# Performance work log

Hardware: AMD Instinct MI355X
Metric: run time of the kernel (lower is better)

Reference implementation:

```python
import jax, jax.numpy as jnp
import numpy as np

B, L, DIM = 4, 2048, 512
H, D = 8, 64
SCALE = D ** -0.5
NEG = -10000.0


def setup_inputs() -> dict:
    key = jax.random.key(0)
    ks = jax.random.split(key, 5)
    std = 1.0 / np.sqrt(DIM)
    return {
        "x": jax.random.normal(ks[0], (B, L, DIM), dtype=jnp.float32),
        "wq": jax.random.normal(ks[1], (H * D, DIM), dtype=jnp.float32) * std,
        "wk": jax.random.normal(ks[2], (H * D, DIM), dtype=jnp.float32) * std,
        "wv": jax.random.normal(ks[3], (H * D, DIM), dtype=jnp.float32) * std,
        "wo": jax.random.normal(ks[4], (DIM, H * D), dtype=jnp.float32) * std,
    }


def reference(x, wq, wk, wv, wo):
    b, l, _ = x.shape
    # projections (torch Linear: y = x @ W.T), split heads -> [b,h,l,d]
    q = (x @ wq.T).reshape(b, l, H, D).transpose(0, 2, 1, 3)
    k = (x @ wk.T).reshape(b, l, H, D).transpose(0, 2, 1, 3)
    v = (x @ wv.T).reshape(b, l, H, D).transpose(0, 2, 1, 3)
    scores = jnp.einsum("bhld,bhsd->bhls", q, k) * SCALE
    scores = jnp.nan_to_num(scores, nan=0.0, posinf=10000.0, neginf=NEG)
    diag = jnp.eye(l, dtype=bool)[None, None]  # [1,1,l,l]
    scores = jnp.where(diag, NEG, scores)
    attn = jax.nn.softmax(scores, axis=-1)
    attn = jnp.where(diag, 0.0, attn)
    attn = jnp.nan_to_num(attn, nan=0.0, posinf=0.0, neginf=0.0)
    out = jnp.einsum("bhls,bhsd->bhld", attn, v)
    out = out.transpose(0, 2, 1, 3).reshape(b, l, H * D)
    return out @ wo.T
```

## Files before the change

### kernel.cpp

```cpp
#include <hip/hip_runtime.h>
#include <hip/hip_bf16.h>


#define Bsz 4
#define Lsz 2048
#define DIMsz 512
#define Hsz 8
#define Dsz 64

typedef _Float16 f16;
typedef __attribute__((ext_vector_type(8))) _Float16 f16x8;
typedef __attribute__((ext_vector_type(4))) _Float16 f16x4;
typedef __attribute__((ext_vector_type(2))) __fp16 fp16x2;
typedef __attribute__((ext_vector_type(4))) float f32x4;
typedef __attribute__((ext_vector_type(16))) float f32x16;
typedef unsigned int u32;
typedef __attribute__((ext_vector_type(2))) unsigned int u32x2;

#if __has_builtin(__builtin_amdgcn_exp2f)
#define EXP2(x) __builtin_amdgcn_exp2f(x)
#else
#define EXP2(x) __expf(0.6931471805599453f * (x))
#endif

__device__ __forceinline__ u32 pack2(float a, float b) {
#if __has_builtin(__builtin_amdgcn_cvt_pkrtz)
    fp16x2 h = __builtin_amdgcn_cvt_pkrtz(a, b);
    return __builtin_bit_cast(u32, h);
#else
    fp16x2 h; h.x = (__fp16)a; h.y = (__fp16)b;
    return __builtin_bit_cast(u32, h);
#endif
}

#if __has_builtin(__builtin_amdgcn_permlane32_swap)
__device__ __forceinline__ void plswap(u32& a, u32& b) {
    u32x2 r = __builtin_amdgcn_permlane32_swap(a, b, false, false);
    a = r.x; b = r.y;
}
#else
__device__ __forceinline__ void plswap(u32& a, u32& b) {
    u32 sa = (u32)__shfl_xor((int)a, 32);
    u32 sb = (u32)__shfl_xor((int)b, 32);
    bool hi = (threadIdx.x & 32) != 0;
    u32 na = hi ? sb : a;
    u32 nb = hi ? b : sa;
    a = na; b = nb;
}
#endif

__device__ __forceinline__ void gl2lds16(const void* g, void* l) {
    __builtin_amdgcn_global_load_lds(
        (const __attribute__((address_space(1))) u32*)g,
        (__attribute__((address_space(3))) u32*)l, 16, 0, 0);
}

__global__ __launch_bounds__(256) void pack_f16(
    const float* __restrict__ x, const float* __restrict__ wq,
    const float* __restrict__ wk, const float* __restrict__ wv,
    const float* __restrict__ wo,
    f16* __restrict__ xh, f16* __restrict__ w3h, f16* __restrict__ woh)
{
    int bx = blockIdx.x, seg, blk;
    if (bx < 4096) { seg = 0; blk = bx; }
    else { seg = 1 + ((bx - 4096) >> 8); blk = (bx - 4096) & 255; }
    const float* s; f16* d; float sc = 1.0f;
    switch (seg) {
        case 0: s = x;  d = xh;            break;
        case 1: s = wq; d = w3h;           sc = 0.18033688011112042f; break;
        case 2: s = wk; d = w3h + 262144;  break;
        case 3: s = wv; d = w3h + 524288;  break;
        default: s = wo; d = woh;          break;
    }
    int i = (blk * 256 + threadIdx.x) * 4;
    float4 v = *(const float4*)(s + i);
    f16x4 o;
    o.x = (f16)(v.x * sc); o.y = (f16)(v.y * sc);
    o.z = (f16)(v.z * sc); o.w = (f16)(v.w * sc);
    *(f16x4*)(d + i) = o;
}

__global__ __launch_bounds__(256) void gemm_qkv_f16(
    const f16* __restrict__ A, const f16* __restrict__ B,
    f16* __restrict__ qh, f16* __restrict__ kh, f16* __restrict__ vth)
{
    __shared__ __align__(16) char smem[32768];
    f16* Ash = (f16*)smem;
    f16* Bsh = (f16*)(smem + 16384);

    const int tid = threadIdx.x;
    const int w = tid >> 6, lane = tid & 63;
    const int quad = lane >> 4, low = lane & 15;
    const int wm = w >> 1, wn = w & 1;
    const int m0 = blockIdx.y * 128, n0 = blockIdx.x * 128;

    f32x4 acc[4][4];
    #pragma unroll
    for (int i = 0; i < 4; i++)
        #pragma unroll
        for (int j = 0; j < 4; j++) acc[i][j] = (f32x4){0.f, 0.f, 0.f, 0.f};

    #pragma unroll 1
    for (int k0 = 0; k0 < DIMsz; k0 += 64) {
        __syncthreads();
        #pragma unroll
        for (int j = 0; j < 4; j++) {
            int t = j * 256 + tid;
            int r = t >> 3, g = t & 7;
            int gc = (g ^ (r & 7)) * 8;
            char* lb = (char*)Ash + (j * 256 + w * 64) * 16;
            gl2lds16(A + (size_t)(m0 + r) * DIMsz + k0 + gc, lb);
            char* lb2 = (char*)Bsh + (j * 256 + w * 64) * 16;
            gl2lds16(B + (size_t)(n0 + r) * DIMsz + k0 + gc, lb2);
        }
        __syncthreads();

        #pragma unroll
        for (int ks2 = 0; ks2 < 2; ks2++) {
            f16x8 af[4], bf[4];
            #pragma unroll
            for (int mt = 0; mt < 4; mt++) {
                int ar = wm * 64 + mt * 16 + low;
                int c = ks2 * 4 + quad;
                af[mt] = *(const f16x8*)&Ash[ar * 64 + ((c ^ (ar & 7)) << 3)];
            }
            #pragma unroll
            for (int nt = 0; nt < 4; nt++) {
                int br = wn * 64 + nt * 16 + low;
                int c = ks2 * 4 + quad;
                bf[nt] = *(const f16x8*)&Bsh[br * 64 + ((c ^ (br & 7)) << 3)];
            }
            #pragma unroll
            for (int mt = 0; mt < 4; mt++)
                #pragma unroll
                for (int nt = 0; nt < 4; nt++)
                    acc[mt][nt] = __builtin_amdgcn_mfma_f32_16x16x32_f16(
                        af[mt], bf[nt], acc[mt][nt], 0, 0, 0);
        }
    }

    const int proj = n0 >> 9;
    const int b_ = m0 >> 11, l0 = m0 & (Lsz - 1);
    if (proj < 2) {
        f16* dst = (proj == 0) ? qh : kh;
        f16* Tq = (f16*)smem;
        const int hb = (n0 & 511) >> 6;
        #pragma unroll 1
        for (int hs = 0; hs < 2; hs++) {
            __syncthreads();
            if (wn == hs) {
                #pragma unroll
                for (int nt = 0; nt < 4; nt++) {
                    int cl = nt * 16 + low;
                    #pragma unroll
                    for (int mt = 0; mt < 4; mt++)
                        #pragma unroll
                        for (int r = 0; r < 4; r++) {
                            int l = wm * 64 + mt * 16 + quad * 4 + r;
                            Tq[l * 72 + cl] = (f16)acc[mt][nt][r];
                        }
                }
            }
            __syncthreads();
            int l = tid >> 1, d0 = (tid & 1) * 32;
            size_t bhh = (size_t)(b_ * Hsz + hb + hs);
            f16* dstp = dst + (bhh * Lsz + l0 + l) * Dsz + d0;
            const f16* srcp = Tq + l * 72 + d0;
            #pragma unroll
            for (int j = 0; j < 4; j++)
                *(f16x8*)(dstp + j * 8) = *(const f16x8*)(srcp + j * 8);
        }
    } else {
        const int hb = (n0 & 511) >> 6;
        f16* Tv = (f16*)smem;
        #pragma unroll 1
        for (int hs = 0; hs < 2; hs++) {
            __syncthreads();
            if (wn == hs) {
                #pragma unroll
                for (int nt = 0; nt < 4; nt++) {
                    int d = nt * 16 + low;
                    #pragma unroll
                    for (int mt = 0; mt < 4; mt++)
                        #pragma unroll
                        for (int r = 0; r < 4; r++) {
                            int l = wm * 64 + mt * 16 + quad * 4 + r;
                            Tv[d * 136 + l] = (f16)acc[mt][nt][r];
                        }
                }
            }
            __syncthreads();
            int d = tid >> 2, seg = tid & 3;
            size_t bh = (size_t)(b_ * Hsz + hb + hs);
            f16* dstp = vth + (bh * 64 + d) * (size_t)Lsz + l0 + seg * 32;
            const f16* srcp = Tv + d * 136 + seg * 32;
            #pragma unroll
            for (int j = 0; j < 4; j++)
                *(f16x8*)(dstp + j * 8) = *(const f16x8*)(srcp + j * 8);
        }
    }
}

__global__ __launch_bounds__(256, 4) void attn_mfma(
    const f16* __restrict__ q, const f16* __restrict__ k,
    const f16* __restrict__ vt, f16* __restrict__ ctx)
{
    __shared__ __align__(16) char smem[33792];

    const int tid = threadIdx.x;
    const int w = tid >> 6, lane = tid & 63;
    const int col = lane & 31;
    const int h = lane >> 5;
    const int kw = w & 1, qw = w >> 1;
    const int bh = blockIdx.x;
    const int qb = blockIdx.y;
    const int q0 = qb * 64;
    const size_t kvb = (size_t)bh * Lsz;

    f16* Ks = (f16*)smem;
    f16* Vs = (f16*)(smem + 16384);

    f16x8 qf[4];
    #pragma unroll
    for (int s = 0; s < 4; s++)
        qf[s] = *(const f16x8*)(q + (kvb + q0 + qw * 32 + col) * Dsz
                                  + s * 16 + h * 8);
    #pragma unroll
    for (int s = 0; s < 4; s++)
        asm volatile("" :: "v"(qf[s]));

    const f16* kp; const f16* vp;
    {
        int r8 = tid >> 3, g8 = tid & 7;
        int gc = (g8 ^ (r8 & 7) ^ ((r8 >> 3) & 3)) << 3;
        kp = k + (kvb + r8) * Dsz + gc;
        vp = vt + ((size_t)bh * Dsz + r8) * Lsz + gc;
    }
    char* kl = (char*)smem + w * 1024;
    char* vl = (char*)smem + 16384 + w * 1024;

    const int cswz = (col & 7) ^ ((col >> 3) & 3);
    const f16* kfp[4];
    #pragma unroll
    for (int s = 0; s < 4; s++)
        kfp[s] = Ks + (kw * 32 + col) * 64 + (((s * 2 + h) ^ cswz) << 3);
    const f16* vfp[2][2];
    #pragma unroll
    for (int dt = 0; dt < 2; dt++)
        #pragma unroll
        for (int ks = 0; ks < 2; ks++) {
            int cv = kw * 4 + ks * 2 + h;
            vfp[dt][ks] = Vs + (dt * 32 + col) * 64 + ((cv ^ cswz) << 3);
        }

    f32x16 acc[2];
    #pragma unroll
    for (int dt = 0; dt < 2; dt++)
        #pragma unroll
        for (int i = 0; i < 16; i++) acc[dt][i] = 0.f;
    float lsum = 0.f;

    gl2lds16(kp,            kl);
    gl2lds16(kp + 32 * Dsz, kl + 4096);
    gl2lds16(vp,            vl);
    gl2lds16(vp + 32 * Lsz, vl + 4096);
    kp += 64 * Dsz;
    vp += 64;

#define ATTN_ROUND(S0, P, PRE) do {                                           \
    const int ko_ = (P) * 8192;                                               \
    if (PRE) {                                                                \
        const int nx_ = ((P) ^ 1) * 8192;                                     \
        gl2lds16(kp,            kl + nx_);                                    \
        gl2lds16(kp + 32 * Dsz, kl + nx_ + 4096);                             \
        gl2lds16(vp,            vl + nx_);                                    \
        gl2lds16(vp + 32 * Lsz, vl + nx_ + 4096);                             \
        kp += 64 * Dsz;                                                       \
        vp += 64;                                                             \
        asm volatile("s_waitcnt vmcnt(4)" ::: "memory");                      \
    } else {                                                                  \
        asm volatile("s_waitcnt vmcnt(0)" ::: "memory");                      \
    }                                                                         \
    __builtin_amdgcn_s_barrier();                                             \
    __builtin_amdgcn_sched_barrier(0);                                        \
      \
    f32x16 st;                                                                \
    _Pragma("unroll")                                                         \
    for (int i = 0; i < 16; i++) st[i] = 0.f;                                 \
    __builtin_amdgcn_s_setprio(1);                                            \
    _Pragma("unroll")                                                         \
    for (int s = 0; s < 4; s++) {                                             \
        f16x8 kf = *(const f16x8*)((const char*)kfp[s] + ko_);                \
        st = __builtin_amdgcn_mfma_f32_32x32x16_f16(kf, qf[s], st, 0, 0, 0);  \
    }                                                                         \
    __builtin_amdgcn_s_setprio(0);                                            \
                \
    _Pragma("unroll")                                                         \
    for (int i = 0; i < 16; i++) st[i] = EXP2(st[i]);                         \
    if ((S0) == q0 && kw == qw) {                                             \
        _Pragma("unroll")                                                     \
        for (int i = 0; i < 16; i++) {                                        \
            int row = (i & 3) + 8 * (i >> 2) + 4 * h;                         \
            st[i] = (row == col) ? 0.f : st[i];                               \
        }                                                                     \
    }                                                                         \
    _Pragma("unroll")                                                         \
    for (int i = 0; i < 16; i++) lsum += st[i];                               \
                                                \
    u32 P2[8];                                                                \
    _Pragma("unroll")                                                         \
    for (int j = 0; j < 8; j++)                                               \
        P2[j] = pack2(st[2 * j], st[2 * j + 1]);                              \
    plswap(P2[0], P2[2]); plswap(P2[1], P2[3]);                               \
    plswap(P2[4], P2[6]); plswap(P2[5], P2[7]);                               \
    union { u32 u[4]; f16x8 v; } pfa, pfb;                                    \
    _Pragma("unroll")                                                         \
    for (int jj = 0; jj < 4; jj++) {                                          \
        pfa.u[jj] = P2[jj];                                                   \
        pfb.u[jj] = P2[4 + jj];                                               \
    }                                                                         \
                               \
    __builtin_amdgcn_s_setprio(1);                                            \
    _Pragma("unroll")                                                         \
    for (int dt = 0; dt < 2; dt++) {                                          \
        f16x8 vf0 = *(const f16x8*)((const char*)vfp[dt][0] + ko_);           \
        acc[dt] = __builtin_amdgcn_mfma_f32_32x32x16_f16(                     \
            vf0, pfa.v, acc[dt], 0, 0, 0);                                    \
        f16x8 vf1 = *(const f16x8*)((const char*)vfp[dt][1] + ko_);           \
        acc[dt] = __builtin_amdgcn_mfma_f32_32x32x16_f16(                     \
            vf1, pfb.v, acc[dt], 0, 0, 0);                                    \
    }                                                                         \
    __builtin_amdgcn_s_setprio(0);                                            \
    __builtin_amdgcn_sched_barrier(0);                                        \
    __builtin_amdgcn_s_barrier();                                             \
} while (0)

    #pragma unroll 1
    for (int s0 = 0; s0 < Lsz; s0 += 128) {
        ATTN_ROUND(s0, 0, true);
        ATTN_ROUND(s0 + 64, 1, (s0 + 128 < Lsz));
    }
#undef ATTN_ROUND

    __syncthreads();

    float* Lsp = (float*)(smem + 32768);
    lsum += __shfl_xor(lsum, 32);
    if (h == 0) Lsp[qw * 64 + kw * 32 + col] = lsum;

    float* Om = (float*)smem;
    if (kw == 1) {
        float* og = Om + qw * 2048;
        #pragma unroll
        for (int dt = 0; dt < 2; dt++)
            #pragma unroll
            for (int i = 0; i < 16; i++) {
                int row = (i & 3) + 8 * (i >> 2) + 4 * h;
                og[(dt * 32 + row) * 32 + col] = acc[dt][i];
            }
    }
    __syncthreads();
    if (kw == 0) {
        const float* og = Om + qw * 2048;
        #pragma unroll
        for (int dt = 0; dt < 2; dt++)
            #pragma unroll
            for (int i = 0; i < 16; i++) {
                int row = (i & 3) + 8 * (i >> 2) + 4 * h;
                acc[dt][i] += og[(dt * 32 + row) * 32 + col];
            }
        const int b = bh >> 3, hh = bh & 7;
        float ls = Lsp[qw * 64 + col] + Lsp[qw * 64 + 32 + col];
        const float inv = 1.0f / ls;
        f16* op = ctx + ((size_t)(b * Lsz + q0 + qw * 32 + col)) * DIMsz
                      + hh * 64;
        #pragma unroll
        for (int dt = 0; dt < 2; dt++)
            #pragma unroll
            for (int r4 = 0; r4 < 4; r4++) {
                f16x4 o;
                o.x = (f16)(acc[dt][4 * r4 + 0] * inv);
                o.y = (f16)(acc[dt][4 * r4 + 1] * inv);
                o.z = (f16)(acc[dt][4 * r4 + 2] * inv);
                o.w = (f16)(acc[dt][4 * r4 + 3] * inv);
                *(f16x4*)(op + dt * 32 + 8 * r4 + 4 * h) = o;
            }
    }
}

__global__ __launch_bounds__(256) void gemm_out_f16(
    const f16* __restrict__ A, const f16* __restrict__ B,
    float* __restrict__ C)
{
    __shared__ f16 Ash[64 * 64];
    __shared__ f16 Bsh[64 * 64];
    const int tid = threadIdx.x;
    const int w = tid >> 6, lane = tid & 63;
    const int quad = lane >> 4, low = lane & 15;
    const int wm = w >> 1, wn = w & 1;
    const int m0 = blockIdx.y * 64, n0 = blockIdx.x * 64;

    f32x4 acc[2][2];
    #pragma unroll
    for (int i = 0; i < 2; i++)
        #pragma unroll
        for (int j = 0; j < 2; j++) acc[i][j] = (f32x4){0.f, 0.f, 0.f, 0.f};

    #pragma unroll 1
    for (int k0 = 0; k0 < DIMsz; k0 += 64) {
        __syncthreads();
        #pragma unroll
        for (int j = 0; j < 2; j++) {
            int t = j * 256 + tid;
            int r = t >> 3, g = t & 7;
            int gc = (g ^ (r & 7)) * 8;
            char* lb = (char*)Ash + (j * 256 + w * 64) * 16;
            gl2lds16(A + (size_t)(m0 + r) * DIMsz + k0 + gc, lb);
            char* lb2 = (char*)Bsh + (j * 256 + w * 64) * 16;
            gl2lds16(B + (size_t)(n0 + r) * DIMsz + k0 + gc, lb2);
        }
        __syncthreads();

        #pragma unroll
        for (int ks2 = 0; ks2 < 2; ks2++) {
            f16x8 af[2], bf[2];
            #pragma unroll
            for (int mt = 0; mt < 2; mt++) {
                int ar = wm * 32 + mt * 16 + low;
                int c = ks2 * 4 + quad;
                af[mt] = *(const f16x8*)&Ash[ar * 64 + ((c ^ (ar & 7)) << 3)];
            }
            #pragma unroll
            for (int nt = 0; nt < 2; nt++) {
                int br = wn * 32 + nt * 16 + low;
                int c = ks2 * 4 + quad;
                bf[nt] = *(const f16x8*)&Bsh[br * 64 + ((c ^ (br & 7)) << 3)];
            }
            #pragma unroll
            for (int mt = 0; mt < 2; mt++)
                #pragma unroll
                for (int nt = 0; nt < 2; nt++)
                    acc[mt][nt] = __builtin_amdgcn_mfma_f32_16x16x32_f16(
                        af[mt], bf[nt], acc[mt][nt], 0, 0, 0);
        }
    }

    #pragma unroll
    for (int mt = 0; mt < 2; mt++)
        #pragma unroll
        for (int r = 0; r < 4; r++) {
            int m = m0 + wm * 32 + mt * 16 + quad * 4 + r;
            #pragma unroll
            for (int nt = 0; nt < 2; nt++) {
                int n = n0 + wn * 32 + nt * 16 + low;
                C[(size_t)m * DIMsz + n] = acc[mt][nt][r];
            }
        }
}

extern "C" void kernel_launch(void* const* d_in, const int* in_sizes, int n_in,
                              void* d_out, int out_size, void* d_ws, size_t ws_size,
                              hipStream_t stream) {
    const float* x  = (const float*)d_in[0];
    const float* wq = (const float*)d_in[1];
    const float* wk = (const float*)d_in[2];
    const float* wv = (const float*)d_in[3];
    const float* wo = (const float*)d_in[4];
    float* out = (float*)d_out;

    const size_t NTOK = (size_t)Bsz * Lsz;
    const size_t XSZ  = NTOK * DIMsz;

    f16* xh   = (f16*)d_ws;
    f16* w3h  = xh + XSZ;
    f16* woh  = w3h + 3 * 262144;
    f16* qh   = woh + 262144;
    f16* kh   = qh + XSZ;
    f16* vth  = kh + XSZ;
    f16* ctxh = vth + XSZ;

    pack_f16<<<5120, 256, 0, stream>>>(x, wq, wk, wv, wo, xh, w3h, woh);

    dim3 g1(1536 / 128, NTOK / 128);
    gemm_qkv_f16<<<g1, 256, 0, stream>>>(xh, w3h, qh, kh, vth);

    dim3 g2(Bsz * Hsz, Lsz / 64);
    attn_mfma<<<g2, 256, 0, stream>>>(qh, kh, vth, ctxh);

    dim3 g3(DIMsz / 64, NTOK / 64);
    gemm_out_f16<<<g3, 256, 0, stream>>>(ctxh, woh, out);
}
```

Before: 162.9 us.

## Double-buffer LDS in QKV and output projection GEMMs with async prefetch

Both projection GEMMs now use two LDS buffers and prefetch the next K-tile via global-to-LDS loads while computing the current one. Explicit vmcnt waits and raw s_barrier replace the per-iteration __syncthreads pair. Address computation is hoisted out of the loop and MFMA blocks are wrapped in s_setprio. This is meant to hide global-load latency in the GEMMs. In exchange, LDS usage doubles (64KB for the QKV kernel), which may lower occupancy.

```diff
diff --git a/kernel.cpp b/kernel.cpp
--- a/kernel.cpp
+++ b/kernel.cpp
@@ -84,10 +84,7 @@
     const f16* __restrict__ A, const f16* __restrict__ B,
     f16* __restrict__ qh, f16* __restrict__ kh, f16* __restrict__ vth)
 {
-    __shared__ __align__(16) char smem[32768];
-    f16* Ash = (f16*)smem;
-    f16* Bsh = (f16*)(smem + 16384);
-
+    __shared__ __align__(16) char smem[65536];
     const int tid = threadIdx.x;
     const int w = tid >> 6, lane = tid & 63;
     const int quad = lane >> 4, low = lane & 15;
@@ -100,44 +97,72 @@
         #pragma unroll
         for (int j = 0; j < 4; j++) acc[i][j] = (f32x4){0.f, 0.f, 0.f, 0.f};
 
+    const f16* ap; const f16* bp;
+    {
+        int r8 = tid >> 3, g8 = tid & 7;
+        int gc = (g8 ^ (r8 & 7)) << 3;
+        ap = A + (size_t)(m0 + r8) * DIMsz + gc;
+        bp = B + (size_t)(n0 + r8) * DIMsz + gc;
+    }
+    char* al = (char*)smem + w * 1024;
+    char* bl = (char*)smem + 16384 + w * 1024;
+
+#define QKV_STAGE(POFF) do {                                                  \
+    _Pragma("unroll")                                                         \
+    for (int j = 0; j < 4; j++) {                                             \
+        gl2lds16(ap + (size_t)j * 32 * DIMsz, al + (POFF) + j * 4096);        \
+        gl2lds16(bp + (size_t)j * 32 * DIMsz, bl + (POFF) + j * 4096);        \
+    }                                                                         \
+    ap += 64; bp += 64;                                                       \
+} while (0)
+
+    QKV_STAGE(0);
+
     #pragma unroll 1
-    for (int k0 = 0; k0 < DIMsz; k0 += 64) {
-        __syncthreads();
-        #pragma unroll
-        for (int j = 0; j < 4; j++) {
-            int t = j * 256 + tid;
-            int r = t >> 3, g = t & 7;
-            int gc = (g ^ (r & 7)) * 8;
-            char* lb = (char*)Ash + (j * 256 + w * 64) * 16;
-            gl2lds16(A + (size_t)(m0 + r) * DIMsz + k0 + gc, lb);
-            char* lb2 = (char*)Bsh + (j * 256 + w * 64) * 16;
-            gl2lds16(B + (size_t)(n0 + r) * DIMsz + k0 + gc, lb2);
+    for (int k2 = 0; k2 < 4; k2++) {
+        #pragma unroll
+        for (int pp = 0; pp < 2; pp++) {
+            const int po = pp * 32768;
+            const bool pre = (k2 * 2 + pp) < 7;
+            if (pre) {
+                QKV_STAGE((pp ^ 1) * 32768);
+                asm volatile("s_waitcnt vmcnt(8)" ::: "memory");
+            } else {
+                asm volatile("s_waitcnt vmcnt(0)" ::: "memory");
+            }
+            __builtin_amdgcn_s_barrier();
+            __builtin_amdgcn_sched_barrier(0);
+            const f16* Ash = (const f16*)(smem + po);
+            const f16* Bsh = (const f16*)(smem + po + 16384);
+            #pragma unroll
+            for (int ks2 = 0; ks2 < 2; ks2++) {
+                f16x8 af[4], bf[4];
+                #pragma unroll
+                for (int mt = 0; mt < 4; mt++) {
+                    int ar = wm * 64 + mt * 16 + low;
+                    int c = ks2 * 4 + quad;
+                    af[mt] = *(const f16x8*)&Ash[ar * 64 + ((c ^ (ar & 7)) << 3)];
+                }
+                #pragma unroll
+                for (int nt = 0; nt < 4; nt++) {
+                    int br = wn * 64 + nt * 16 + low;
+                    int c = ks2 * 4 + quad;
+                    bf[nt] = *(const f16x8*)&Bsh[br * 64 + ((c ^ (br & 7)) << 3)];
+                }
+                __builtin_amdgcn_s_setprio(1);
+                #pragma unroll
+                for (int mt = 0; mt < 4; mt++)
+                    #pragma unroll
+                    for (int nt = 0; nt < 4; nt++)
+                        acc[mt][nt] = __builtin_amdgcn_mfma_f32_16x16x32_f16(
+                            af[mt], bf[nt], acc[mt][nt], 0, 0, 0);
+                __builtin_amdgcn_s_setprio(0);
+            }
+            __builtin_amdgcn_sched_barrier(0);
+            __builtin_amdgcn_s_barrier();
         }
-        __syncthreads();
-
-        #pragma unroll
-        for (int ks2 = 0; ks2 < 2; ks2++) {
-            f16x8 af[4], bf[4];
-            #pragma unroll
-            for (int mt = 0; mt < 4; mt++) {
-                int ar = wm * 64 + mt * 16 + low;
-                int c = ks2 * 4 + quad;
-                af[mt] = *(const f16x8*)&Ash[ar * 64 + ((c ^ (ar & 7)) << 3)];
-            }
-            #pragma unroll
-            for (int nt = 0; nt < 4; nt++) {
-                int br = wn * 64 + nt * 16 + low;
-                int c = ks2 * 4 + quad;
-                bf[nt] = *(const f16x8*)&Bsh[br * 64 + ((c ^ (br & 7)) << 3)];
-            }
-            #pragma unroll
-            for (int mt = 0; mt < 4; mt++)
-                #pragma unroll
-                for (int nt = 0; nt < 4; nt++)
-                    acc[mt][nt] = __builtin_amdgcn_mfma_f32_16x16x32_f16(
-                        af[mt], bf[nt], acc[mt][nt], 0, 0, 0);
-        }
-    }
+    }
+#undef QKV_STAGE
 
     const int proj = n0 >> 9;
     const int b_ = m0 >> 11, l0 = m0 & (Lsz - 1);
@@ -392,8 +417,7 @@
     const f16* __restrict__ A, const f16* __restrict__ B,
     float* __restrict__ C)
 {
-    __shared__ f16 Ash[64 * 64];
-    __shared__ f16 Bsh[64 * 64];
+    __shared__ __align__(16) char smem[32768];
     const int tid = threadIdx.x;
     const int w = tid >> 6, lane = tid & 63;
     const int quad = lane >> 4, low = lane & 15;
@@ -406,44 +430,72 @@
         #pragma unroll
         for (int j = 0; j < 2; j++) acc[i][j] = (f32x4){0.f, 0.f, 0.f, 0.f};
 
+    const f16* ap; const f16* bp;
+    {
+        int r8 = tid >> 3, g8 = tid & 7;
+        int gc = (g8 ^ (r8 & 7)) << 3;
+        ap = A + (size_t)(m0 + r8) * DIMsz + gc;
+        bp = B + (size_t)(n0 + r8) * DIMsz + gc;
+    }
+    char* al = (char*)smem + w * 1024;
+    char* bl = (char*)smem + 8192 + w * 1024;
+
+#define OUT_STAGE(POFF) do {                                                  \
+    _Pragma("unroll")                                                         \
+    for (int j = 0; j < 2; j++) {                                             \
+        gl2lds16(ap + (size_t)j * 32 * DIMsz, al + (POFF) + j * 4096);        \
+        gl2lds16(bp + (size_t)j * 32 * DIMsz, bl + (POFF) + j * 4096);        \
+    }                                                                         \
+    ap += 64; bp += 64;                                                       \
+} while (0)
+
+    OUT_STAGE(0);
+
     #pragma unroll 1
-    for (int k0 = 0; k0 < DIMsz; k0 += 64) {
-        __syncthreads();
-        #pragma unroll
-        for (int j = 0; j < 2; j++) {
-            int t = j * 256 + tid;
-            int r = t >> 3, g = t & 7;
-            int gc = (g ^ (r & 7)) * 8;
-            char* lb = (char*)Ash + (j * 256 + w * 64) * 16;
-            gl2lds16(A + (size_t)(m0 + r) * DIMsz + k0 + gc, lb);
-            char* lb2 = (char*)Bsh + (j * 256 + w * 64) * 16;
-            gl2lds16(B + (size_t)(n0 + r) * DIMsz + k0 + gc, lb2);
+    for (int k2 = 0; k2 < 4; k2++) {
+        #pragma unroll
+        for (int pp = 0; pp < 2; pp++) {
+            const int po = pp * 16384;
+            const bool pre = (k2 * 2 + pp) < 7;
+            if (pre) {
+                OUT_STAGE((pp ^ 1) * 16384);
+                asm volatile("s_waitcnt vmcnt(4)" ::: "memory");
+            } else {
+                asm volatile("s_waitcnt vmcnt(0)" ::: "memory");
+            }
+            __builtin_amdgcn_s_barrier();
+            __builtin_amdgcn_sched_barrier(0);
+            const f16* Ash = (const f16*)(smem + po);
+            const f16* Bsh = (const f16*)(smem + po + 8192);
+            #pragma unroll
+            for (int ks2 = 0; ks2 < 2; ks2++) {
+                f16x8 af[2], bf[2];
+                #pragma unroll
+                for (int mt = 0; mt < 2; mt++) {
+                    int ar = wm * 32 + mt * 16 + low;
+                    int c = ks2 * 4 + quad;
+                    af[mt] = *(const f16x8*)&Ash[ar * 64 + ((c ^ (ar & 7)) << 3)];
+                }
+                #pragma unroll
+                for (int nt = 0; nt < 2; nt++) {
+                    int br = wn * 32 + nt * 16 + low;
+                    int c = ks2 * 4 + quad;
+                    bf[nt] = *(const f16x8*)&Bsh[br * 64 + ((c ^ (br & 7)) << 3)];
+                }
+                __builtin_amdgcn_s_setprio(1);
+                #pragma unroll
+                for (int mt = 0; mt < 2; mt++)
+                    #pragma unroll
+                    for (int nt = 0; nt < 2; nt++)
+                        acc[mt][nt] = __builtin_amdgcn_mfma_f32_16x16x32_f16(
+                            af[mt], bf[nt], acc[mt][nt], 0, 0, 0);
+                __builtin_amdgcn_s_setprio(0);
+            }
+            __builtin_amdgcn_sched_barrier(0);
+            __builtin_amdgcn_s_barrier();
         }
-        __syncthreads();
-
-        #pragma unroll
-        for (int ks2 = 0; ks2 < 2; ks2++) {
-            f16x8 af[2], bf[2];
-            #pragma unroll
-            for (int mt = 0; mt < 2; mt++) {
-                int ar = wm * 32 + mt * 16 + low;
-                int c = ks2 * 4 + quad;
-                af[mt] = *(const f16x8*)&Ash[ar * 64 + ((c ^ (ar & 7)) << 3)];
-            }
-            #pragma unroll
-            for (int nt = 0; nt < 2; nt++) {
-                int br = wn * 32 + nt * 16 + low;
-                int c = ks2 * 4 + quad;
-                bf[nt] = *(const f16x8*)&Bsh[br * 64 + ((c ^ (br & 7)) << 3)];
-            }
-            #pragma unroll
-            for (int mt = 0; mt < 2; mt++)
-                #pragma unroll
-                for (int nt = 0; nt < 2; nt++)
-                    acc[mt][nt] = __builtin_amdgcn_mfma_f32_16x16x32_f16(
-                        af[mt], bf[nt], acc[mt][nt], 0, 0, 0);
-        }
-    }
+    }
+#undef OUT_STAGE
 
     #pragma unroll
     for (int mt = 0; mt < 2; mt++)
```

Result: no change. 164.4 us (+1.0%).
